# Kernel tuning notes

Hardware: AMD Instinct MI355X
Metric: run time of the kernel (lower is better)

## Reference

```python
import jax, jax.numpy as jnp
import numpy as np
from jax import lax

N, E = 100000, 1600000
IN_DIM, EDGE_DIM, HIDDEN, LAYERS, HEADS, OUT_DIM = 16, 4, 128, 6, 8, 3
C = HIDDEN // HEADS  # per-head dim
EPS = 1e-5


def setup_inputs() -> dict:
    key = jax.random.key(0)
    ks = jax.random.split(key, 24)
    s = 0.1
    inp = {
        "x": jax.random.normal(ks[0], (N, IN_DIM), jnp.float32),
        "edge_index": jax.random.randint(ks[1], (2, E), 0, N, jnp.int32),
        "edge_attr": jax.random.normal(ks[2], (E, EDGE_DIM), jnp.float32),
        # input projection
        "W_in": s * jax.random.normal(ks[3], (IN_DIM, HIDDEN), jnp.float32),
        "b_in": jnp.zeros((HIDDEN,), jnp.float32),
        "ln_in_g": jnp.ones((HIDDEN,), jnp.float32),
        "ln_in_b": jnp.zeros((HIDDEN,), jnp.float32),
        # stacked GAT layer params [L, ...]
        "Wg": s * jax.random.normal(ks[4], (LAYERS, HIDDEN, HIDDEN), jnp.float32),
        "att_src": s * jax.random.normal(ks[5], (LAYERS, HEADS, C), jnp.float32),
        "att_dst": s * jax.random.normal(ks[6], (LAYERS, HEADS, C), jnp.float32),
        "We": s * jax.random.normal(ks[7], (LAYERS, EDGE_DIM, HIDDEN), jnp.float32),
        "att_edge": s * jax.random.normal(ks[8], (LAYERS, HEADS, C), jnp.float32),
        "bg": jnp.zeros((LAYERS, HIDDEN), jnp.float32),
        "ln_g": jnp.ones((LAYERS, HIDDEN), jnp.float32),
        "ln_b": jnp.zeros((LAYERS, HIDDEN), jnp.float32),
        # output head
        "W1": s * jax.random.normal(ks[9], (HIDDEN, HIDDEN), jnp.float32),
        "b1": jnp.zeros((HIDDEN,), jnp.float32),
        "W2": s * jax.random.normal(ks[10], (HIDDEN, OUT_DIM), jnp.float32),
        "b2": jnp.zeros((OUT_DIM,), jnp.float32),
    }
    return inp


def layer_norm(x, g, b):
    mu = jnp.mean(x, axis=-1, keepdims=True)
    var = jnp.var(x, axis=-1, keepdims=True)
    return (x - mu) * lax.rsqrt(var + EPS) * g + b


def gat_block(h, src, dst, edge_attr, Wg, a_s, a_d, We, a_e, bg, g, b):
    # linear projection, shared for src/dst (same input set in PyG GATConv)
    hp = (h @ Wg).reshape(N, HEADS, C)                  # [N,H,C]
    alpha_src = jnp.sum(hp * a_s, axis=-1)              # [N,H]
    alpha_dst = jnp.sum(hp * a_d, axis=-1)              # [N,H]
    ep = (edge_attr @ We).reshape(E, HEADS, C)          # [E,H,C]
    alpha_e = jnp.sum(ep * a_e, axis=-1)                # [E,H]
    # edge-wise attention logits, leaky_relu slope 0.2 (PyG default)
    alpha = jax.nn.leaky_relu(alpha_src[src] + alpha_dst[dst] + alpha_e, 0.2)
    # segment softmax over incoming edges of each dst node
    m = jax.ops.segment_max(alpha, dst, num_segments=N)  # [N,H]
    m = jnp.where(jnp.isfinite(m), m, 0.0)
    a = jnp.exp(alpha - m[dst])
    denom = jax.ops.segment_sum(a, dst, num_segments=N)  # [N,H]
    a = a / (denom[dst] + 1e-16)
    # weighted message aggregation
    msg = hp[src] * a[:, :, None]                        # [E,H,C]
    out = jax.ops.segment_sum(msg, dst, num_segments=N).reshape(N, HIDDEN) + bg
    # residual + LayerNorm (dropout inactive in eval)
    return layer_norm(h + out, g, b)


def reference(x, edge_index, edge_attr, W_in, b_in, ln_in_g, ln_in_b,
              Wg, att_src, att_dst, We, att_edge, bg, ln_g, ln_b,
              W1, b1, W2, b2):
    src, dst = edge_index[0], edge_index[1]
    h = layer_norm(jax.nn.relu(x @ W_in + b_in), ln_in_g, ln_in_b)

    def body(h, p):
        Wg_i, as_i, ad_i, We_i, ae_i, bg_i, g_i, b_i = p
        return gat_block(h, src, dst, edge_attr, Wg_i, as_i, ad_i, We_i, ae_i, bg_i, g_i, b_i), None

    h, _ = lax.scan(body, h, (Wg, att_src, att_dst, We, att_edge, bg, ln_g, ln_b))
    h = jax.nn.relu(h @ W1 + b1)
    return jax.nn.relu(h @ W2 + b2)
```

## Files before the change

kernel.cpp:

```cpp
#include <hip/hip_runtime.h>
#include <hip/hip_bf16.h>

#define NN 100000
#define NE 1600000
#define HID 128
#define NH 8
#define HC 16
#define NL 6
#define CAP 64

typedef unsigned int u32;
typedef __attribute__((ext_vector_type(4))) float f32x4;
typedef __attribute__((ext_vector_type(8))) short bf16x8;

__device__ __forceinline__ float u2f(unsigned short v){
  union{u32 i; float f;} c; c.i = ((u32)v) << 16; return c.f;
}
__device__ __forceinline__ float lo2f(u32 u){ union{u32 i; float f;} c; c.i = u << 16; return c.f; }
__device__ __forceinline__ float hi2f(u32 u){ union{u32 i; float f;} c; c.i = u & 0xFFFF0000u; return c.f; }
__device__ __forceinline__ unsigned short f2bf(float f){
  u32 u = __float_as_uint(f);
  u = (u + 0x7FFFu + ((u >> 16) & 1u)) >> 16;
  return (unsigned short)u;
}

__device__ __forceinline__ float ldw(const void* p, long long i, int fl){
  if (fl) return ((const float*)p)[i];
  return u2f(((const unsigned short*)p)[i]);
}

__global__ void sniff_k(const void* g, int* flag){
  if (threadIdx.x == 0 && blockIdx.x == 0){
    const unsigned short* p = (const unsigned short*)g;
    flag[0] = (p[0] == 0x3F80) ? 0 : 1;
  }
}

__global__ void zero_k(int* p, int n){
  int i = blockIdx.x*256 + threadIdx.x;
  if (i < n) p[i] = 0;
}

#define PF_TOT 4355
__global__ void prep_params_k(const void* att_src, const void* att_dst,
    const void* bg, const void* ln_g, const void* ln_b, const void* b1,
    const void* W2, const void* b2, float* __restrict__ pf, const int* flag){
  int fl = flag[0];
  int i = blockIdx.x*256 + threadIdx.x;
  if (i >= PF_TOT) return;
  float v;
  if (i < 768)       v = ldw(att_src, i, fl);
  else if (i < 1536) v = ldw(att_dst, i-768, fl);
  else if (i < 2304) v = ldw(bg, i-1536, fl);
  else if (i < 3072) v = ldw(ln_g, i-2304, fl);
  else if (i < 3840) v = ldw(ln_b, i-3072, fl);
  else if (i < 3968) v = ldw(b1, i-3840, fl);
  else if (i < 4352) v = ldw(W2, i-3968, fl);
  else               v = ldw(b2, i-4352, fl);
  pf[i] = v;
}

__global__ __launch_bounds__(256) void prep_wb_k(const void* Wg, const void* W1,
    unsigned short* __restrict__ wB, const int* flag){
  int fl = flag[0];
  int i = blockIdx.x*256 + threadIdx.x;
  if (i >= 7*HID*HID) return;
  int l = i >> 14, r = i & 16383;
  int n = r >> 7, k = r & 127;
  float v = (l < 6) ? ldw(Wg, (long long)l*HID*HID + k*HID + n, fl)
                    : ldw(W1, (long long)k*HID + n, fl);
  int ks = (((k >> 3) ^ (n & 7)) << 3) | (k & 7);
  wB[(long long)l*HID*HID + n*HID + ks] = f2bf(v);
}

__global__ void prep_wae_k(const void* We, const void* ae, float* __restrict__ Wae,
                           const int* flag){
  int fl = flag[0];
  int id = threadIdx.x;
  if (id >= NL*4*NH) return;
  int l = id / 32, r = id % 32, d = r / 8, hh = r % 8;
  float s = 0.f;
  #pragma unroll
  for (int c = 0; c < HC; ++c)
    s += ldw(We, l*4*HID + d*HID + hh*HC + c, fl) * ldw(ae, l*NH*HC + hh*HC + c, fl);
  Wae[id] = s;
}

__global__ __launch_bounds__(256) void inproj_k(const void* x,
    const void* W_in, const void* b_in, const void* g, const void* b,
    float* __restrict__ h, const int* flag){
  __shared__ float xs[2][16];
  __shared__ float r1[2][2], r2[2][2];
  int fl = flag[0];
  int half = threadIdx.x >> 7;
  int t = threadIdx.x & 127;
  long long n = (long long)blockIdx.x*2 + half;
  if (t < 16) xs[half][t] = ldw(x, n*16 + t, fl);
  __syncthreads();
  float acc = ldw(b_in, t, fl);
  #pragma unroll
  for (int k = 0; k < 16; ++k) acc = fmaf(xs[half][k], ldw(W_in, k*HID + t, fl), acc);
  acc = fmaxf(acc, 0.f);
  float s1 = acc, s2 = acc*acc;
  #pragma unroll
  for (int off = 32; off; off >>= 1){ s1 += __shfl_xor(s1, off); s2 += __shfl_xor(s2, off); }
  if ((t & 63) == 0){ r1[half][t>>6] = s1; r2[half][t>>6] = s2; }
  __syncthreads();
  float S1 = r1[half][0] + r1[half][1], S2 = r2[half][0] + r2[half][1];
  float mu = S1 * (1.f/128.f);
  float var = S2 * (1.f/128.f) - mu*mu;
  float rr = rsqrtf(var + 1e-5f);
  h[n*HID + t] = (acc - mu) * rr * ldw(g, t, fl) + ldw(b, t, fl);
}

__global__ __launch_bounds__(256) void count_k(const int* __restrict__ dst,
    int* __restrict__ deg, int* __restrict__ pos){
  int e = blockIdx.x*256 + threadIdx.x;
  if (e >= NE) return;
  pos[e] = atomicAdd(&deg[dst[e]], 1);
}
__global__ __launch_bounds__(256) void scan_block_k(const int* __restrict__ in,
    int* __restrict__ out, int* __restrict__ bsum, int n){
  __shared__ int lds[256];
  int t = threadIdx.x, i = blockIdx.x*256 + t;
  int v = (i < n) ? in[i] : 0;
  lds[t] = v;
  __syncthreads();
  #pragma unroll
  for (int off = 1; off < 256; off <<= 1){
    int tmp = (t >= off) ? lds[t-off] : 0;
    __syncthreads();
    lds[t] += tmp;
    __syncthreads();
  }
  int incl = lds[t];
  if (i < n) out[i] = incl - v;
  if (t == 255) bsum[blockIdx.x] = incl;
}
__global__ __launch_bounds__(512) void scan_top_k(const int* __restrict__ bsum,
    int* __restrict__ boff, int nb){
  __shared__ int lds[512];
  int t = threadIdx.x;
  int v = (t < nb) ? bsum[t] : 0;
  lds[t] = v;
  __syncthreads();
  #pragma unroll
  for (int off = 1; off < 512; off <<= 1){
    int tmp = (t >= off) ? lds[t-off] : 0;
    __syncthreads();
    lds[t] += tmp;
    __syncthreads();
  }
  boff[t] = lds[t] - v;
}
__global__ __launch_bounds__(256) void scan_add_k(int* __restrict__ rowptr,
    const int* __restrict__ boff, int n){
  int i = blockIdx.x*256 + threadIdx.x;
  if (i < n) rowptr[i] += boff[i >> 8];
  if (i == 0) rowptr[n] = NE;
}
__global__ __launch_bounds__(256) void scatter_k(const int* __restrict__ src,
    const int* __restrict__ dst, const int* __restrict__ rowptr,
    const int* __restrict__ pos, const void* eattr,
    uint4* __restrict__ pk, const int* flag){
  int fl = flag[0];
  int e = blockIdx.x*256 + threadIdx.x;
  if (e >= NE) return;
  int d = dst[e];
  int i = rowptr[d] + pos[e];
  uint4 o;
  o.x = (u32)src[e];
  if (fl){
    float4 v = *(const float4*)((const float*)eattr + (long long)e*4);
    o.y = ((u32)f2bf(v.y) << 16) | (u32)f2bf(v.x);
    o.z = ((u32)f2bf(v.w) << 16) | (u32)f2bf(v.z);
  } else {
    uint2 er = *(const uint2*)((const unsigned short*)eattr + (long long)e*4);
    o.y = er.x; o.z = er.y;
  }
  o.w = 0;
  pk[i] = o;
}

__global__ __launch_bounds__(256) void gemm_mfma_k(const float* __restrict__ A,
    const unsigned short* __restrict__ wBl, unsigned short* __restrict__ Cout,
    const float* __restrict__ biasF, int relu,
    const float* __restrict__ attS, const float* __restrict__ attD,
    float* __restrict__ asrc, float* __restrict__ adst){
  __shared__ unsigned short smem[2*HID*HID];
  unsigned short* As = smem;
  unsigned short* Bs = smem + HID*HID;
  int t = threadIdx.x;
  int row0 = blockIdx.x * 128;

  {
    const uint4* srcp = (const uint4*)wBl;
    uint4* dstp = (uint4*)Bs;
    #pragma unroll
    for (int i = 0; i < 8; ++i) dstp[i*256 + t] = srcp[i*256 + t];
  }
  {
    int r = t >> 1, kh = (t & 1) * 64;
    int arow = row0 + r;
    float a64[64];
    if (arow < NN){
      const float* ap = A + (long long)arow*HID + kh;
      #pragma unroll
      for (int i = 0; i < 16; ++i){
        float4 q = *(const float4*)(ap + 4*i);
        a64[4*i] = q.x; a64[4*i+1] = q.y; a64[4*i+2] = q.z; a64[4*i+3] = q.w;
      }
    } else {
      #pragma unroll
      for (int i = 0; i < 64; ++i) a64[i] = 0.f;
    }
    #pragma unroll
    for (int g = 0; g < 8; ++g){
      int gg = (kh >> 3) + g;
      u32 wp[4];
      #pragma unroll
      for (int p = 0; p < 4; ++p)
        wp[p] = ((u32)f2bf(a64[g*8 + 2*p + 1]) << 16) | (u32)f2bf(a64[g*8 + 2*p]);
      uint4 q; q.x = wp[0]; q.y = wp[1]; q.z = wp[2]; q.w = wp[3];
      *(uint4*)&As[r*HID + ((gg ^ (r & 7)) << 3)] = q;
    }
  }
  __syncthreads();

  int l = t & 63, wv = t >> 6;
  int wr = wv >> 1, wc = wv & 1;
  int lr = l & 15, lg = l >> 4;
  f32x4 acc[4][4] = {};
  #pragma unroll
  for (int kk = 0; kk < 4; ++kk){
    bf16x8 af[4], bfr[4];
    int grp = kk*4 + lg;
    #pragma unroll
    for (int m = 0; m < 4; ++m){
      int row = wr*64 + m*16 + lr;
      af[m] = *(const bf16x8*)&As[row*HID + ((grp ^ (row & 7)) << 3)];
    }
    #pragma unroll
    for (int n = 0; n < 4; ++n){
      int col = wc*64 + n*16 + lr;
      bfr[n] = *(const bf16x8*)&Bs[col*HID + ((grp ^ (col & 7)) << 3)];
    }
    #pragma unroll
    for (int m = 0; m < 4; ++m){
      #pragma unroll
      for (int n = 0; n < 4; ++n){
        asm volatile("v_mfma_f32_16x16x32_bf16 %0, %1, %2, %0"
                     : "+v"(acc[m][n]) : "v"(af[m]), "v"(bfr[n]));
      }
    }
  }
  __syncthreads();

  unsigned short* Cl = smem;
  #pragma unroll
  for (int m = 0; m < 4; ++m){
    #pragma unroll
    for (int n = 0; n < 4; ++n){
      int col = wc*64 + n*16 + lr;
      float bv = biasF ? biasF[col] : 0.f;
      #pragma unroll
      for (int j = 0; j < 4; ++j){
        int row = wr*64 + m*16 + lg*4 + j;
        float v = acc[m][n][j] + bv;
        if (relu) v = fmaxf(v, 0.f);
        Cl[row*136 + col] = f2bf(v);
      }
    }
  }
  __syncthreads();

  {
    int r = t >> 1, kh = (t & 1)*64;
    if (row0 + r < NN){
      const uint4* srcp = (const uint4*)&Cl[r*136 + kh];
      uint4* dstp = (uint4*)(Cout + (long long)(row0 + r)*HID + kh);
      #pragma unroll
      for (int i = 0; i < 8; ++i) dstp[i] = srcp[i];
    }
  }
  if (attS){
    int hh = t & 7;
    float avS[16], avD[16];
    #pragma unroll
    for (int c = 0; c < 16; ++c){ avS[c] = attS[hh*16 + c]; avD[c] = attD[hh*16 + c]; }
    #pragma unroll
    for (int q = 0; q < 4; ++q){
      int r = q*32 + (t >> 3);
      int rr = row0 + r;
      if (rr < NN){
        const unsigned short* cp = &Cl[r*136 + hh*16];
        uint4 q0 = *(const uint4*)cp;
        uint4 q1 = *(const uint4*)(cp + 8);
        u32 uu[8] = {q0.x,q0.y,q0.z,q0.w,q1.x,q1.y,q1.z,q1.w};
        float sS = 0.f, sD = 0.f;
        #pragma unroll
        for (int p = 0; p < 8; ++p){
          float h0 = lo2f(uu[p]), h1 = hi2f(uu[p]);
          sS = fmaf(h0, avS[2*p], sS); sS = fmaf(h1, avS[2*p+1], sS);
          sD = fmaf(h0, avD[2*p], sD); sD = fmaf(h1, avD[2*p+1], sD);
        }
        asrc[(long long)rr*NH + hh] = sS;
        adst[(long long)rr*NH + hh] = sD;
      }
    }
  }
}

__global__ __launch_bounds__(256) void gat_node_k(const int* __restrict__ rowptr,
    const uint4* __restrict__ pk,
    const float* __restrict__ Wae_l, const float* __restrict__ asrc,
    const float* __restrict__ adst, const unsigned short* __restrict__ hp,
    float* __restrict__ h, const float* __restrict__ bgF,
    const float* __restrict__ gF, const float* __restrict__ bF){
  __shared__ float lw[4][CAP][8];
  __shared__ int   ls[4][CAP];
  int wv = threadIdx.x >> 6, l = threadIdx.x & 63;
  int n = blockIdx.x*4 + wv;
  int b0 = rowptr[n], b1 = rowptr[n+1];
  int deg = b1 - b0;
  int sub = l >> 3, hh = l & 7;
  float wae0 = Wae_l[hh], wae1 = Wae_l[8+hh], wae2 = Wae_l[16+hh], wae3 = Wae_l[24+hh];
  float adn = adst[n*NH + hh];
  float den = 0.f;
  for (int i = b0 + sub; i < b1; i += 8){
    uint4 q = pk[i];
    int s = (int)q.x;
    float v = asrc[s*NH + hh] + adn;
    v = fmaf(lo2f(q.y), wae0, v);
    v = fmaf(hi2f(q.y), wae1, v);
    v = fmaf(lo2f(q.z), wae2, v);
    v = fmaf(hi2f(q.z), wae3, v);
    v = fmaxf(v, 0.2f*v);
    float w = __expf(v);
    int idx = i - b0;
    if (idx < CAP){
      lw[wv][idx][hh] = w;
      if (hh == 0) ls[wv][idx] = s;
    }
    den += w;
  }
  den += __shfl_xor(den, 8);
  den += __shfl_xor(den, 16);
  den += __shfl_xor(den, 32);
  int eg = l >> 4, cl = l & 15;
  int hd = cl >> 1;
  float rden = 1.f / (__shfl(den, hd) + 1e-16f);
  const unsigned short* hpc = hp + 8*cl;
  float a[8] = {0,0,0,0,0,0,0,0};
  int cap_end = b0 + (deg < CAP ? deg : CAP);
  int i = b0;
  for (; i + 8 <= cap_end; i += 8){
    int j0 = i + eg, j1 = i + 4 + eg;
    int s0 = ls[wv][j0 - b0], s1v = ls[wv][j1 - b0];
    float w0 = lw[wv][j0 - b0][hd], w1 = lw[wv][j1 - b0][hd];
    uint4 q0 = *(const uint4*)(hpc + (long long)s0*HID);
    uint4 q1 = *(const uint4*)(hpc + (long long)s1v*HID);
    a[0] = fmaf(w0, lo2f(q0.x), a[0]); a[1] = fmaf(w0, hi2f(q0.x), a[1]);
    a[2] = fmaf(w0, lo2f(q0.y), a[2]); a[3] = fmaf(w0, hi2f(q0.y), a[3]);
    a[4] = fmaf(w0, lo2f(q0.z), a[4]); a[5] = fmaf(w0, hi2f(q0.z), a[5]);
    a[6] = fmaf(w0, lo2f(q0.w), a[6]); a[7] = fmaf(w0, hi2f(q0.w), a[7]);
    a[0] = fmaf(w1, lo2f(q1.x), a[0]); a[1] = fmaf(w1, hi2f(q1.x), a[1]);
    a[2] = fmaf(w1, lo2f(q1.y), a[2]); a[3] = fmaf(w1, hi2f(q1.y), a[3]);
    a[4] = fmaf(w1, lo2f(q1.z), a[4]); a[5] = fmaf(w1, hi2f(q1.z), a[5]);
    a[6] = fmaf(w1, lo2f(q1.w), a[6]); a[7] = fmaf(w1, hi2f(q1.w), a[7]);
  }
  for (; i < cap_end; i += 4){
    int j = i + eg;
    if (j < cap_end){
      int s = ls[wv][j - b0];
      float w = lw[wv][j - b0][hd];
      uint4 q = *(const uint4*)(hpc + (long long)s*HID);
      a[0] = fmaf(w, lo2f(q.x), a[0]); a[1] = fmaf(w, hi2f(q.x), a[1]);
      a[2] = fmaf(w, lo2f(q.y), a[2]); a[3] = fmaf(w, hi2f(q.y), a[3]);
      a[4] = fmaf(w, lo2f(q.z), a[4]); a[5] = fmaf(w, hi2f(q.z), a[5]);
      a[6] = fmaf(w, lo2f(q.w), a[6]); a[7] = fmaf(w, hi2f(q.w), a[7]);
    }
  }
  if (deg > CAP){
    float w0c = Wae_l[hd], w1c = Wae_l[8+hd], w2c = Wae_l[16+hd], w3c = Wae_l[24+hd];
    float adc = adst[n*NH + hd];
    for (int j = cap_end + eg; j < b1; j += 4){
      uint4 e4 = pk[j];
      int s = (int)e4.x;
      float v = asrc[s*NH + hd] + adc;
      v = fmaf(lo2f(e4.y), w0c, v);
      v = fmaf(hi2f(e4.y), w1c, v);
      v = fmaf(lo2f(e4.z), w2c, v);
      v = fmaf(hi2f(e4.z), w3c, v);
      v = fmaxf(v, 0.2f*v);
      float w = __expf(v);
      uint4 q = *(const uint4*)(hpc + (long long)s*HID);
      a[0] = fmaf(w, lo2f(q.x), a[0]); a[1] = fmaf(w, hi2f(q.x), a[1]);
      a[2] = fmaf(w, lo2f(q.y), a[2]); a[3] = fmaf(w, hi2f(q.y), a[3]);
      a[4] = fmaf(w, lo2f(q.z), a[4]); a[5] = fmaf(w, hi2f(q.z), a[5]);
      a[6] = fmaf(w, lo2f(q.w), a[6]); a[7] = fmaf(w, hi2f(q.w), a[7]);
    }
  }
  #pragma unroll
  for (int j = 0; j < 8; ++j){
    a[j] += __shfl_xor(a[j], 16);
    a[j] += __shfl_xor(a[j], 32);
  }
  const float* hrow = h + (long long)n*HID + 8*cl;
  float4 hv0 = *(const float4*)hrow;
  float4 hv1 = *(const float4*)(hrow + 4);
  float hv[8] = {hv0.x,hv0.y,hv0.z,hv0.w,hv1.x,hv1.y,hv1.z,hv1.w};
  float tv[8];
  float s1 = 0.f, s2 = 0.f;
  #pragma unroll
  for (int j = 0; j < 8; ++j){
    tv[j] = hv[j] + a[j]*rden + bgF[8*cl + j];
    s1 += tv[j]; s2 += tv[j]*tv[j];
  }
  s1 += __shfl_xor(s1, 1); s2 += __shfl_xor(s2, 1);
  s1 += __shfl_xor(s1, 2); s2 += __shfl_xor(s2, 2);
  s1 += __shfl_xor(s1, 4); s2 += __shfl_xor(s2, 4);
  s1 += __shfl_xor(s1, 8); s2 += __shfl_xor(s2, 8);
  float mu = s1 * (1.f/128.f);
  float var = s2 * (1.f/128.f) - mu*mu;
  float rr = rsqrtf(var + 1e-5f);
  if (eg == 0){
    float4 o0, o1;
    o0.x = (tv[0]-mu)*rr*gF[8*cl+0] + bF[8*cl+0];
    o0.y = (tv[1]-mu)*rr*gF[8*cl+1] + bF[8*cl+1];
    o0.z = (tv[2]-mu)*rr*gF[8*cl+2] + bF[8*cl+2];
    o0.w = (tv[3]-mu)*rr*gF[8*cl+3] + bF[8*cl+3];
    o1.x = (tv[4]-mu)*rr*gF[8*cl+4] + bF[8*cl+4];
    o1.y = (tv[5]-mu)*rr*gF[8*cl+5] + bF[8*cl+5];
    o1.z = (tv[6]-mu)*rr*gF[8*cl+6] + bF[8*cl+6];
    o1.w = (tv[7]-mu)*rr*gF[8*cl+7] + bF[8*cl+7];
    *(float4*)(h + (long long)n*HID + 8*cl) = o0;
    *(float4*)(h + (long long)n*HID + 8*cl + 4) = o1;
  }
}

__global__ __launch_bounds__(256) void head2_k(const unsigned short* __restrict__ hp,
    const float* __restrict__ W2F, const float* __restrict__ b2F, void* out,
    const int* flag){
  int fl = flag[0];
  int n = blockIdx.x*4 + (threadIdx.x >> 6);
  if (n >= NN) return;
  int l = threadIdx.x & 63;
  u32 u = *(const u32*)(hp + (long long)n*HID + 2*l);
  float p0 = lo2f(u), p1 = hi2f(u);
  int c0 = 2*l, c1 = 2*l + 1;
  float o0 = p0*W2F[c0*3+0] + p1*W2F[c1*3+0];
  float o1 = p0*W2F[c0*3+1] + p1*W2F[c1*3+1];
  float o2 = p0*W2F[c0*3+2] + p1*W2F[c1*3+2];
  #pragma unroll
  for (int off = 32; off; off >>= 1){
    o0 += __shfl_xor(o0, off); o1 += __shfl_xor(o1, off); o2 += __shfl_xor(o2, off);
  }
  if (l == 0){
    float r0 = fmaxf(o0 + b2F[0], 0.f);
    float r1 = fmaxf(o1 + b2F[1], 0.f);
    float r2 = fmaxf(o2 + b2F[2], 0.f);
    if (fl){
      float* o = (float*)out;
      o[n*3+0] = r0; o[n*3+1] = r1; o[n*3+2] = r2;
    } else {
      unsigned short* o = (unsigned short*)out;
      o[n*3+0] = f2bf(r0); o[n*3+1] = f2bf(r1); o[n*3+2] = f2bf(r2);
    }
  }
}

extern "C" void kernel_launch(void* const* d_in, const int* in_sizes, int n_in,
                              void* d_out, int out_size, void* d_ws, size_t ws_size,
                              hipStream_t stream){
  const void* x       = d_in[0];
  const int*  eidx    = (const int*)d_in[1];
  const void* eattr   = d_in[2];
  const void* W_in    = d_in[3];
  const void* b_in    = d_in[4];
  const void* ln_in_g = d_in[5];
  const void* ln_in_b = d_in[6];
  const void* Wg      = d_in[7];
  const void* att_src = d_in[8];
  const void* att_dst = d_in[9];
  const void* We      = d_in[10];
  const void* att_e   = d_in[11];
  const void* bg      = d_in[12];
  const void* ln_g    = d_in[13];
  const void* ln_b    = d_in[14];
  const void* W1      = d_in[15];
  const void* b1v     = d_in[16];
  const void* W2      = d_in[17];
  const void* b2      = d_in[18];

  char* ws = (char*)d_ws;
  size_t off = 0;
  auto alloc = [&](size_t bytes) -> void* {
    void* p = ws + off; off += (bytes + 255) & ~(size_t)255; return p;
  };
  float*  h     = (float*) alloc((size_t)NN*HID*4);
  unsigned short* hp = (unsigned short*)alloc((size_t)NN*HID*2);
  float*  asrc  = (float*) alloc((size_t)NN*NH*4);
  float*  adst  = (float*) alloc((size_t)NN*NH*4);
  float*  Wae   = (float*) alloc(NL*32*4);
  float*  pf    = (float*) alloc(PF_TOT*4);
  unsigned short* wB = (unsigned short*)alloc((size_t)7*HID*HID*2);
  int* deg      = (int*)   alloc((size_t)NN*4);
  int* pos      = (int*)   alloc((size_t)NE*4);
  int* rowptr   = (int*)   alloc((size_t)(NN+1)*4);
  int* bsum     = (int*)   alloc(512*4);
  int* boffp    = (int*)   alloc(512*4);
  uint4* pk     = (uint4*) alloc((size_t)NE*16);
  int* flag     = (int*)   alloc(256);

  const int* src = eidx;
  const int* dst = eidx + NE;
  int nb = (NN + 255) / 256;

  sniff_k<<<1, 64, 0, stream>>>(ln_in_g, flag);
  zero_k<<<nb, 256, 0, stream>>>(deg, NN);
  prep_wae_k<<<1, 256, 0, stream>>>(We, att_e, Wae, flag);
  prep_params_k<<<(PF_TOT+255)/256, 256, 0, stream>>>(att_src, att_dst, bg, ln_g, ln_b,
                                                      b1v, W2, b2, pf, flag);
  prep_wb_k<<<(7*HID*HID+255)/256, 256, 0, stream>>>(Wg, W1, wB, flag);
  inproj_k<<<NN/2, 256, 0, stream>>>(x, W_in, b_in, ln_in_g, ln_in_b, h, flag);
  count_k<<<(NE+255)/256, 256, 0, stream>>>(dst, deg, pos);
  scan_block_k<<<nb, 256, 0, stream>>>(deg, rowptr, bsum, NN);
  scan_top_k<<<1, 512, 0, stream>>>(bsum, boffp, nb);
  scan_add_k<<<nb, 256, 0, stream>>>(rowptr, boffp, NN);
  scatter_k<<<(NE+255)/256, 256, 0, stream>>>(src, dst, rowptr, pos, eattr, pk, flag);

  const float* attS = pf;
  const float* attD = pf + 768;
  const float* bgF  = pf + 1536;
  const float* gF   = pf + 2304;
  const float* bF   = pf + 3072;
  const float* b1F  = pf + 3840;
  const float* W2F  = pf + 3968;
  const float* b2F  = pf + 4352;

  int gblocks = (NN + 127) / 128;
  for (int l = 0; l < NL; ++l){
    gemm_mfma_k<<<gblocks, 256, 0, stream>>>(h, wB + (size_t)l*HID*HID, hp,
                                             nullptr, 0, attS + l*128, attD + l*128,
                                             asrc, adst);
    gat_node_k<<<NN/4, 256, 0, stream>>>(rowptr, pk, Wae + l*32, asrc, adst,
                                         hp, h, bgF + l*128, gF + l*128, bF + l*128);
  }
  gemm_mfma_k<<<gblocks, 256, 0, stream>>>(h, wB + (size_t)6*HID*HID, hp, b1F, 1,
                                           nullptr, nullptr, nullptr, nullptr);
  head2_k<<<(NN+3)/4, 256, 0, stream>>>(hp, W2F, b2F, d_out, flag);
}
```

Before: 1.049 ms.

## Stream GEMM B fragments from global with prefetch; unroll GAT edge loops

```diff
diff --git a/kernel.cpp b/kernel.cpp
--- a/kernel.cpp
+++ b/kernel.cpp
@@ -69,8 +69,7 @@
   int n = r >> 7, k = r & 127;
   float v = (l < 6) ? ldw(Wg, (long long)l*HID*HID + k*HID + n, fl)
                     : ldw(W1, (long long)k*HID + n, fl);
-  int ks = (((k >> 3) ^ (n & 7)) << 3) | (k & 7);
-  wB[(long long)l*HID*HID + n*HID + ks] = f2bf(v);
+  wB[(long long)l*HID*HID + n*HID + k] = f2bf(v);
 }
 
 __global__ void prep_wae_k(const void* We, const void* ae, float* __restrict__ Wae,
@@ -187,71 +186,70 @@
     const float* __restrict__ biasF, int relu,
     const float* __restrict__ attS, const float* __restrict__ attD,
     float* __restrict__ asrc, float* __restrict__ adst){
-  __shared__ unsigned short smem[2*HID*HID];
+  __shared__ unsigned short smem[HID*136];
   unsigned short* As = smem;
-  unsigned short* Bs = smem + HID*HID;
   int t = threadIdx.x;
   int row0 = blockIdx.x * 128;
-
-  {
-    const uint4* srcp = (const uint4*)wBl;
-    uint4* dstp = (uint4*)Bs;
-    #pragma unroll
-    for (int i = 0; i < 8; ++i) dstp[i*256 + t] = srcp[i*256 + t];
-  }
-  {
-    int r = t >> 1, kh = (t & 1) * 64;
-    int arow = row0 + r;
-    float a64[64];
-    if (arow < NN){
-      const float* ap = A + (long long)arow*HID + kh;
-      #pragma unroll
-      for (int i = 0; i < 16; ++i){
-        float4 q = *(const float4*)(ap + 4*i);
-        a64[4*i] = q.x; a64[4*i+1] = q.y; a64[4*i+2] = q.z; a64[4*i+3] = q.w;
-      }
-    } else {
-      #pragma unroll
-      for (int i = 0; i < 64; ++i) a64[i] = 0.f;
-    }
-    #pragma unroll
-    for (int g = 0; g < 8; ++g){
-      int gg = (kh >> 3) + g;
-      u32 wp[4];
-      #pragma unroll
-      for (int p = 0; p < 4; ++p)
-        wp[p] = ((u32)f2bf(a64[g*8 + 2*p + 1]) << 16) | (u32)f2bf(a64[g*8 + 2*p]);
-      uint4 q; q.x = wp[0]; q.y = wp[1]; q.z = wp[2]; q.w = wp[3];
-      *(uint4*)&As[r*HID + ((gg ^ (r & 7)) << 3)] = q;
-    }
-  }
-  __syncthreads();
-
   int l = t & 63, wv = t >> 6;
   int wr = wv >> 1, wc = wv & 1;
   int lr = l & 15, lg = l >> 4;
+
+  int r = t >> 1, kh = (t & 1) * 64;
+  int arow = row0 + r;
+  float a64[64];
+  if (arow < NN){
+    const float* ap = A + (long long)arow*HID + kh;
+    #pragma unroll
+    for (int i2 = 0; i2 < 16; ++i2){
+      float4 q = *(const float4*)(ap + 4*i2);
+      a64[4*i2] = q.x; a64[4*i2+1] = q.y; a64[4*i2+2] = q.z; a64[4*i2+3] = q.w;
+    }
+  } else {
+    #pragma unroll
+    for (int i2 = 0; i2 < 64; ++i2) a64[i2] = 0.f;
+  }
+  const unsigned short* bp = wBl + (long long)(wc*64 + lr)*HID + lg*8;
+  bf16x8 bcur[4], bnxt[4];
+  #pragma unroll
+  for (int n = 0; n < 4; ++n) bcur[n] = *(const bf16x8*)(bp + n*16*HID);
+  #pragma unroll
+  for (int n = 0; n < 4; ++n) bnxt[n] = *(const bf16x8*)(bp + n*16*HID + 32);
+  #pragma unroll
+  for (int g = 0; g < 8; ++g){
+    int gg = (kh >> 3) + g;
+    u32 wp[4];
+    #pragma unroll
+    for (int p = 0; p < 4; ++p)
+      wp[p] = ((u32)f2bf(a64[g*8 + 2*p + 1]) << 16) | (u32)f2bf(a64[g*8 + 2*p]);
+    uint4 q; q.x = wp[0]; q.y = wp[1]; q.z = wp[2]; q.w = wp[3];
+    *(uint4*)&As[r*HID + ((gg ^ (r & 7)) << 3)] = q;
+  }
+  __syncthreads();
+
   f32x4 acc[4][4] = {};
   #pragma unroll
   for (int kk = 0; kk < 4; ++kk){
-    bf16x8 af[4], bfr[4];
     int grp = kk*4 + lg;
+    bf16x8 af[4];
     #pragma unroll
     for (int m = 0; m < 4; ++m){
-      int row = wr*64 + m*16 + lr;
-      af[m] = *(const bf16x8*)&As[row*HID + ((grp ^ (row & 7)) << 3)];
-    }
-    #pragma unroll
-    for (int n = 0; n < 4; ++n){
-      int col = wc*64 + n*16 + lr;
-      bfr[n] = *(const bf16x8*)&Bs[col*HID + ((grp ^ (col & 7)) << 3)];
+      int rw = wr*64 + m*16 + lr;
+      af[m] = *(const bf16x8*)&As[rw*HID + ((grp ^ (rw & 7)) << 3)];
     }
     #pragma unroll
     for (int m = 0; m < 4; ++m){
       #pragma unroll
       for (int n = 0; n < 4; ++n){
         asm volatile("v_mfma_f32_16x16x32_bf16 %0, %1, %2, %0"
-                     : "+v"(acc[m][n]) : "v"(af[m]), "v"(bfr[n]));
+                     : "+v"(acc[m][n]) : "v"(af[m]), "v"(bcur[n]));
       }
+    }
+    #pragma unroll
+    for (int n = 0; n < 4; ++n) bcur[n] = bnxt[n];
+    if (kk < 2){
+      #pragma unroll
+      for (int n = 0; n < 4; ++n)
+        bnxt[n] = *(const bf16x8*)(bp + n*16*HID + (kk+2)*32);
     }
   }
   __syncthreads();
@@ -275,12 +273,11 @@
   __syncthreads();
 
   {
-    int r = t >> 1, kh = (t & 1)*64;
     if (row0 + r < NN){
       const uint4* srcp = (const uint4*)&Cl[r*136 + kh];
       uint4* dstp = (uint4*)(Cout + (long long)(row0 + r)*HID + kh);
       #pragma unroll
-      for (int i = 0; i < 8; ++i) dstp[i] = srcp[i];
+      for (int i2 = 0; i2 < 8; ++i2) dstp[i2] = srcp[i2];
     }
   }
   if (attS){
@@ -290,10 +287,10 @@
     for (int c = 0; c < 16; ++c){ avS[c] = attS[hh*16 + c]; avD[c] = attD[hh*16 + c]; }
     #pragma unroll
     for (int q = 0; q < 4; ++q){
-      int r = q*32 + (t >> 3);
-      int rr = row0 + r;
+      int rr2 = q*32 + (t >> 3);
+      int rr = row0 + rr2;
       if (rr < NN){
-        const unsigned short* cp = &Cl[r*136 + hh*16];
+        const unsigned short* cp = &Cl[rr2*136 + hh*16];
         uint4 q0 = *(const uint4*)cp;
         uint4 q1 = *(const uint4*)(cp + 8);
         u32 uu[8] = {q0.x,q0.y,q0.z,q0.w,q1.x,q1.y,q1.z,q1.w};
@@ -310,6 +307,12 @@
     }
   }
 }
+
+#define ACC8(wt,qv) \
+  a[0]=fmaf(wt,lo2f((qv).x),a[0]); a[1]=fmaf(wt,hi2f((qv).x),a[1]); \
+  a[2]=fmaf(wt,lo2f((qv).y),a[2]); a[3]=fmaf(wt,hi2f((qv).y),a[3]); \
+  a[4]=fmaf(wt,lo2f((qv).z),a[4]); a[5]=fmaf(wt,hi2f((qv).z),a[5]); \
+  a[6]=fmaf(wt,lo2f((qv).w),a[6]); a[7]=fmaf(wt,hi2f((qv).w),a[7]);
 
 __global__ __launch_bounds__(256) void gat_node_k(const int* __restrict__ rowptr,
     const uint4* __restrict__ pk,
@@ -327,7 +330,31 @@
   float wae0 = Wae_l[hh], wae1 = Wae_l[8+hh], wae2 = Wae_l[16+hh], wae3 = Wae_l[24+hh];
   float adn = adst[n*NH + hh];
   float den = 0.f;
-  for (int i = b0 + sub; i < b1; i += 8){
+  int i = b0 + sub;
+  for (; i + 8 < b1; i += 16){
+    uint4 qa = pk[i];
+    uint4 qb = pk[i+8];
+    int sa = (int)qa.x, sb = (int)qb.x;
+    float va = asrc[sa*NH + hh] + adn;
+    float vb = asrc[sb*NH + hh] + adn;
+    va = fmaf(lo2f(qa.y), wae0, va); vb = fmaf(lo2f(qb.y), wae0, vb);
+    va = fmaf(hi2f(qa.y), wae1, va); vb = fmaf(hi2f(qb.y), wae1, vb);
+    va = fmaf(lo2f(qa.z), wae2, va); vb = fmaf(lo2f(qb.z), wae2, vb);
+    va = fmaf(hi2f(qa.z), wae3, va); vb = fmaf(hi2f(qb.z), wae3, vb);
+    va = fmaxf(va, 0.2f*va); vb = fmaxf(vb, 0.2f*vb);
+    float wa = __expf(va), wb = __expf(vb);
+    int ia = i - b0;
+    if (ia < CAP){
+      lw[wv][ia][hh] = wa;
+      if (hh == 0) ls[wv][ia] = sa;
+    }
+    if (ia + 8 < CAP){
+      lw[wv][ia+8][hh] = wb;
+      if (hh == 0) ls[wv][ia+8] = sb;
+    }
+    den += wa + wb;
+  }
+  if (i < b1){
     uint4 q = pk[i];
     int s = (int)q.x;
     float v = asrc[s*NH + hh] + adn;
@@ -353,21 +380,25 @@
   const unsigned short* hpc = hp + 8*cl;
   float a[8] = {0,0,0,0,0,0,0,0};
   int cap_end = b0 + (deg < CAP ? deg : CAP);
-  int i = b0;
-  for (; i + 8 <= cap_end; i += 8){
-    int j0 = i + eg, j1 = i + 4 + eg;
-    int s0 = ls[wv][j0 - b0], s1v = ls[wv][j1 - b0];
-    float w0 = lw[wv][j0 - b0][hd], w1 = lw[wv][j1 - b0][hd];
+  i = b0;
+  for (; i + 16 <= cap_end; i += 16){
+    int j0 = i + eg - b0, j1 = j0 + 4, j2 = j0 + 8, j3 = j0 + 12;
+    int s0 = ls[wv][j0], s1v = ls[wv][j1], s2v = ls[wv][j2], s3v = ls[wv][j3];
+    float w0 = lw[wv][j0][hd], w1 = lw[wv][j1][hd];
+    float w2 = lw[wv][j2][hd], w3 = lw[wv][j3][hd];
     uint4 q0 = *(const uint4*)(hpc + (long long)s0*HID);
     uint4 q1 = *(const uint4*)(hpc + (long long)s1v*HID);
-    a[0] = fmaf(w0, lo2f(q0.x), a[0]); a[1] = fmaf(w0, hi2f(q0.x), a[1]);
-    a[2] = fmaf(w0, lo2f(q0.y), a[2]); a[3] = fmaf(w0, hi2f(q0.y), a[3]);
-    a[4] = fmaf(w0, lo2f(q0.z), a[4]); a[5] = fmaf(w0, hi2f(q0.z), a[5]);
-    a[6] = fmaf(w0, lo2f(q0.w), a[6]); a[7] = fmaf(w0, hi2f(q0.w), a[7]);
-    a[0] = fmaf(w1, lo2f(q1.x), a[0]); a[1] = fmaf(w1, hi2f(q1.x), a[1]);
-    a[2] = fmaf(w1, lo2f(q1.y), a[2]); a[3] = fmaf(w1, hi2f(q1.y), a[3]);
-    a[4] = fmaf(w1, lo2f(q1.z), a[4]); a[5] = fmaf(w1, hi2f(q1.z), a[5]);
-    a[6] = fmaf(w1, lo2f(q1.w), a[6]); a[7] = fmaf(w1, hi2f(q1.w), a[7]);
+    uint4 q2 = *(const uint4*)(hpc + (long long)s2v*HID);
+    uint4 q3 = *(const uint4*)(hpc + (long long)s3v*HID);
+    ACC8(w0, q0); ACC8(w1, q1); ACC8(w2, q2); ACC8(w3, q3);
+  }
+  for (; i + 8 <= cap_end; i += 8){
+    int j0 = i + eg - b0, j1 = j0 + 4;
+    int s0 = ls[wv][j0], s1v = ls[wv][j1];
+    float w0 = lw[wv][j0][hd], w1 = lw[wv][j1][hd];
+    uint4 q0 = *(const uint4*)(hpc + (long long)s0*HID);
+    uint4 q1 = *(const uint4*)(hpc + (long long)s1v*HID);
+    ACC8(w0, q0); ACC8(w1, q1);
   }
   for (; i < cap_end; i += 4){
     int j = i + eg;
@@ -375,10 +406,7 @@
       int s = ls[wv][j - b0];
       float w = lw[wv][j - b0][hd];
       uint4 q = *(const uint4*)(hpc + (long long)s*HID);
-      a[0] = fmaf(w, lo2f(q.x), a[0]); a[1] = fmaf(w, hi2f(q.x), a[1]);
-      a[2] = fmaf(w, lo2f(q.y), a[2]); a[3] = fmaf(w, hi2f(q.y), a[3]);
-      a[4] = fmaf(w, lo2f(q.z), a[4]); a[5] = fmaf(w, hi2f(q.z), a[5]);
-      a[6] = fmaf(w, lo2f(q.w), a[6]); a[7] = fmaf(w, hi2f(q.w), a[7]);
+      ACC8(w, q);
     }
   }
   if (deg > CAP){
@@ -395,10 +423,7 @@
       v = fmaxf(v, 0.2f*v);
       float w = __expf(v);
       uint4 q = *(const uint4*)(hpc + (long long)s*HID);
-      a[0] = fmaf(w, lo2f(q.x), a[0]); a[1] = fmaf(w, hi2f(q.x), a[1]);
-      a[2] = fmaf(w, lo2f(q.y), a[2]); a[3] = fmaf(w, hi2f(q.y), a[3]);
-      a[4] = fmaf(w, lo2f(q.z), a[4]); a[5] = fmaf(w, hi2f(q.z), a[5]);
-      a[6] = fmaf(w, lo2f(q.w), a[6]); a[7] = fmaf(w, hi2f(q.w), a[7]);
+      ACC8(w, q);
     }
   }
   #pragma unroll
```

Measured after the change: 1.091 ms. 3.9% more time.

## Fuse GAT edge softmax and aggregation into a single pass per node

Applied to the files above, without the earlier changes.

```diff
diff --git a/kernel.cpp b/kernel.cpp
--- a/kernel.cpp
+++ b/kernel.cpp
@@ -7,7 +7,6 @@
 #define NH 8
 #define HC 16
 #define NL 6
-#define CAP 64
 
 typedef unsigned int u32;
 typedef __attribute__((ext_vector_type(4))) float f32x4;
@@ -280,7 +279,7 @@
       const uint4* srcp = (const uint4*)&Cl[r*136 + kh];
       uint4* dstp = (uint4*)(Cout + (long long)(row0 + r)*HID + kh);
       #pragma unroll
-      for (int i = 0; i < 8; ++i) dstp[i] = srcp[i];
+      for (int i2 = 0; i2 < 8; ++i2) dstp[i2] = srcp[i2];
     }
   }
   if (attS){
@@ -290,10 +289,10 @@
     for (int c = 0; c < 16; ++c){ avS[c] = attS[hh*16 + c]; avD[c] = attD[hh*16 + c]; }
     #pragma unroll
     for (int q = 0; q < 4; ++q){
-      int r = q*32 + (t >> 3);
-      int rr = row0 + r;
+      int rr2 = q*32 + (t >> 3);
+      int rr = row0 + rr2;
       if (rr < NN){
-        const unsigned short* cp = &Cl[r*136 + hh*16];
+        const unsigned short* cp = &Cl[rr2*136 + hh*16];
         uint4 q0 = *(const uint4*)cp;
         uint4 q1 = *(const uint4*)(cp + 8);
         u32 uu[8] = {q0.x,q0.y,q0.z,q0.w,q1.x,q1.y,q1.z,q1.w};
@@ -317,90 +316,36 @@
     const float* __restrict__ adst, const unsigned short* __restrict__ hp,
     float* __restrict__ h, const float* __restrict__ bgF,
     const float* __restrict__ gF, const float* __restrict__ bF){
-  __shared__ float lw[4][CAP][8];
-  __shared__ int   ls[4][CAP];
   int wv = threadIdx.x >> 6, l = threadIdx.x & 63;
   int n = blockIdx.x*4 + wv;
   int b0 = rowptr[n], b1 = rowptr[n+1];
-  int deg = b1 - b0;
-  int sub = l >> 3, hh = l & 7;
-  float wae0 = Wae_l[hh], wae1 = Wae_l[8+hh], wae2 = Wae_l[16+hh], wae3 = Wae_l[24+hh];
-  float adn = adst[n*NH + hh];
+  int eg = l >> 4, cl = l & 15;
+  int hd = cl >> 1;
+  float w0c = Wae_l[hd], w1c = Wae_l[8+hd], w2c = Wae_l[16+hd], w3c = Wae_l[24+hd];
+  float adn = adst[n*NH + hd];
+  const unsigned short* hpc = hp + 8*cl;
+  float a[8] = {0,0,0,0,0,0,0,0};
   float den = 0.f;
-  for (int i = b0 + sub; i < b1; i += 8){
-    uint4 q = pk[i];
-    int s = (int)q.x;
-    float v = asrc[s*NH + hh] + adn;
-    v = fmaf(lo2f(q.y), wae0, v);
-    v = fmaf(hi2f(q.y), wae1, v);
-    v = fmaf(lo2f(q.z), wae2, v);
-    v = fmaf(hi2f(q.z), wae3, v);
+  for (int j = b0 + eg; j < b1; j += 4){
+    uint4 e4 = pk[j];
+    int s = (int)e4.x;
+    float v = asrc[s*NH + hd] + adn;
+    v = fmaf(lo2f(e4.y), w0c, v);
+    v = fmaf(hi2f(e4.y), w1c, v);
+    v = fmaf(lo2f(e4.z), w2c, v);
+    v = fmaf(hi2f(e4.z), w3c, v);
     v = fmaxf(v, 0.2f*v);
     float w = __expf(v);
-    int idx = i - b0;
-    if (idx < CAP){
-      lw[wv][idx][hh] = w;
-      if (hh == 0) ls[wv][idx] = s;
-    }
     den += w;
-  }
-  den += __shfl_xor(den, 8);
+    uint4 q = *(const uint4*)(hpc + (long long)s*HID);
+    a[0] = fmaf(w, lo2f(q.x), a[0]); a[1] = fmaf(w, hi2f(q.x), a[1]);
+    a[2] = fmaf(w, lo2f(q.y), a[2]); a[3] = fmaf(w, hi2f(q.y), a[3]);
+    a[4] = fmaf(w, lo2f(q.z), a[4]); a[5] = fmaf(w, hi2f(q.z), a[5]);
+    a[6] = fmaf(w, lo2f(q.w), a[6]); a[7] = fmaf(w, hi2f(q.w), a[7]);
+  }
   den += __shfl_xor(den, 16);
   den += __shfl_xor(den, 32);
-  int eg = l >> 4, cl = l & 15;
-  int hd = cl >> 1;
-  float rden = 1.f / (__shfl(den, hd) + 1e-16f);
-  const unsigned short* hpc = hp + 8*cl;
-  float a[8] = {0,0,0,0,0,0,0,0};
-  int cap_end = b0 + (deg < CAP ? deg : CAP);
-  int i = b0;
-  for (; i + 8 <= cap_end; i += 8){
-    int j0 = i + eg, j1 = i + 4 + eg;
-    int s0 = ls[wv][j0 - b0], s1v = ls[wv][j1 - b0];
-    float w0 = lw[wv][j0 - b0][hd], w1 = lw[wv][j1 - b0][hd];
-    uint4 q0 = *(const uint4*)(hpc + (long long)s0*HID);
-    uint4 q1 = *(const uint4*)(hpc + (long long)s1v*HID);
-    a[0] = fmaf(w0, lo2f(q0.x), a[0]); a[1] = fmaf(w0, hi2f(q0.x), a[1]);
-    a[2] = fmaf(w0, lo2f(q0.y), a[2]); a[3] = fmaf(w0, hi2f(q0.y), a[3]);
-    a[4] = fmaf(w0, lo2f(q0.z), a[4]); a[5] = fmaf(w0, hi2f(q0.z), a[5]);
-    a[6] = fmaf(w0, lo2f(q0.w), a[6]); a[7] = fmaf(w0, hi2f(q0.w), a[7]);
-    a[0] = fmaf(w1, lo2f(q1.x), a[0]); a[1] = fmaf(w1, hi2f(q1.x), a[1]);
-    a[2] = fmaf(w1, lo2f(q1.y), a[2]); a[3] = fmaf(w1, hi2f(q1.y), a[3]);
-    a[4] = fmaf(w1, lo2f(q1.z), a[4]); a[5] = fmaf(w1, hi2f(q1.z), a[5]);
-    a[6] = fmaf(w1, lo2f(q1.w), a[6]); a[7] = fmaf(w1, hi2f(q1.w), a[7]);
-  }
-  for (; i < cap_end; i += 4){
-    int j = i + eg;
-    if (j < cap_end){
-      int s = ls[wv][j - b0];
-      float w = lw[wv][j - b0][hd];
-      uint4 q = *(const uint4*)(hpc + (long long)s*HID);
-      a[0] = fmaf(w, lo2f(q.x), a[0]); a[1] = fmaf(w, hi2f(q.x), a[1]);
-      a[2] = fmaf(w, lo2f(q.y), a[2]); a[3] = fmaf(w, hi2f(q.y), a[3]);
-      a[4] = fmaf(w, lo2f(q.z), a[4]); a[5] = fmaf(w, hi2f(q.z), a[5]);
-      a[6] = fmaf(w, lo2f(q.w), a[6]); a[7] = fmaf(w, hi2f(q.w), a[7]);
-    }
-  }
-  if (deg > CAP){
-    float w0c = Wae_l[hd], w1c = Wae_l[8+hd], w2c = Wae_l[16+hd], w3c = Wae_l[24+hd];
-    float adc = adst[n*NH + hd];
-    for (int j = cap_end + eg; j < b1; j += 4){
-      uint4 e4 = pk[j];
-      int s = (int)e4.x;
-      float v = asrc[s*NH + hd] + adc;
-      v = fmaf(lo2f(e4.y), w0c, v);
-      v = fmaf(hi2f(e4.y), w1c, v);
-      v = fmaf(lo2f(e4.z), w2c, v);
-      v = fmaf(hi2f(e4.z), w3c, v);
-      v = fmaxf(v, 0.2f*v);
-      float w = __expf(v);
-      uint4 q = *(const uint4*)(hpc + (long long)s*HID);
-      a[0] = fmaf(w, lo2f(q.x), a[0]); a[1] = fmaf(w, hi2f(q.x), a[1]);
-      a[2] = fmaf(w, lo2f(q.y), a[2]); a[3] = fmaf(w, hi2f(q.y), a[3]);
-      a[4] = fmaf(w, lo2f(q.z), a[4]); a[5] = fmaf(w, hi2f(q.z), a[5]);
-      a[6] = fmaf(w, lo2f(q.w), a[6]); a[7] = fmaf(w, hi2f(q.w), a[7]);
-    }
-  }
+  float rden = 1.f / (den + 1e-16f);
   #pragma unroll
   for (int j = 0; j < 8; ++j){
     a[j] += __shfl_xor(a[j], 16);
```

New measurement: 1.054 ms. About the same (+0.4%).
